# Kernel optimization log

Hardware: AMD Instinct MI355X
Metric: run time of the kernel (lower is better)

The kernel has to match this reference:

```python
import jax, jax.numpy as jnp
import numpy as np

VOXEL_SIZE = 0.4
PC_START = jnp.array([-75.2, -75.2], dtype=jnp.float32)
GAMMA = 1.1
RADII = (0.8, 1.6)
NSAMPLES = (16, 32)


def _sq_dist(a, b):
    # a:[N,3], b:[N,3] -> [N,N] squared distances (no [N,N,3] intermediate)
    sa = jnp.sum(a * a, axis=-1)
    sb = jnp.sum(b * b, axis=-1)
    return jnp.maximum(sa[:, None] + sb[None, :] - 2.0 * (a @ b.T), 0.0)


def _ball_group(d2, valid, pts, r, k):
    # CUDA ball_query semantics: first-k in-radius neighbor indices (index order),
    # empty slots padded with the first found index (0 if none).
    N = d2.shape[0]
    mask = (d2 < r * r) & valid[None, :]
    skey = jnp.where(mask, jnp.arange(N, dtype=jnp.int32)[None, :], N)
    idx = jnp.sort(skey, axis=-1)[:, :k]            # [N,k]
    first = idx[:, :1]
    idx = jnp.where(idx == N, first, idx)
    idx = jnp.where(idx == N, 0, idx)
    grouped_xyz = pts[idx, :3] - pts[:, None, :3]   # [N,k,3] relative xyz
    return jnp.concatenate([grouped_xyz, pts[idx, 3:5]], axis=-1)  # [N,k,5] (use_xyz)


def _mlp(x, ws, bs):
    for w, b in zip(ws, bs):
        x = jax.nn.relu(x @ w.T + b)
    return x


def _frame(pts, boxes, mlps, num_sample):
    # pts: [N,5] (x,y,z,intensity,time); boxes: [M,7]
    xy = pts[:, :2]
    coords = jnp.floor((xy - PC_START) / VOXEL_SIZE)              # per-point voxel xy coord
    qcoords = jnp.floor((boxes[:, :2] - PC_START) / VOXEL_SIZE)   # box voxel coords
    half_diag = jnp.linalg.norm(boxes[:, 3:5] * 0.5, axis=-1)
    rad_vox = jnp.ceil(half_diag * GAMMA / VOXEL_SIZE)
    dvox = jnp.abs(qcoords[:, None, :] - coords[None, :, :])      # [M,N,2]
    valid = jnp.any(jnp.all(dvox < rad_vox[:, None, None], axis=-1), axis=0)  # [N]

    # cylindrical_pool: per-box top-k points inside cylinder radius
    cur_radiis = half_diag * GAMMA
    dis = jnp.linalg.norm(boxes[:, None, :2] - xy[None, :, :], axis=-1)  # [M,N]
    point_mask = (dis <= cur_radiis[:, None]) & valid[None, :]
    sampled_mask, sampled_idx = jax.lax.top_k(point_mask.astype(pts.dtype), num_sample)

    # PointNet++ SA-MSG evaluated at every point (equivalent to unique->gather in torch src)
    d2 = _sq_dist(pts[:, :3], pts[:, :3])
    feats = [pts[:, :3]]  # use_absolute_xyz: concat query xyz first
    for r, k, (ws, bs) in zip(RADII, NSAMPLES, mlps):
        g = _ball_group(d2, valid, pts, r, k)
        feats.append(jnp.max(_mlp(g, ws, bs), axis=1))  # max-pool over neighbors
    feats = jnp.concatenate(feats, axis=-1)             # [N, 3+32+64]

    sampled_points = pts[sampled_idx] * sampled_mask[..., None]  # zero out-of-radius slots
    return sampled_points, feats[sampled_idx]


def _forward(points, trajectory_rois, params, num_sample):
    B, T, N, C = points.shape
    M = trajectory_rois.shape[2]
    sp, pf = jax.vmap(lambda p, b: _frame(p, b, params, num_sample))(
        points.reshape(B * T, N, C), trajectory_rois.reshape(B * T, M, -1))

    def _merge(x):
        x = x.reshape(B, T, M, num_sample, x.shape[-1])
        return x.transpose(0, 2, 1, 3, 4).reshape(B, M, T * num_sample, x.shape[-1])

    return _merge(sp), _merge(pf)


def setup_inputs():
    key = jax.random.key(0)
    ks = jax.random.split(key, 24)
    B, T, N, M = 2, 4, 4096, 128
    xy = jax.random.uniform(ks[0], (B, T, N, 2), minval=-74.0, maxval=74.0)
    z = jax.random.uniform(ks[1], (B, T, N, 1), minval=-2.0, maxval=4.0)
    inten = jax.random.uniform(ks[2], (B, T, N, 1))
    ts = jnp.broadcast_to(jnp.arange(T, dtype=jnp.float32)[None, :, None, None] * 0.1, (B, T, N, 1))
    points = jnp.concatenate([xy, z, inten, ts], axis=-1)
    bxy = jax.random.uniform(ks[3], (B, T, M, 2), minval=-70.0, maxval=70.0)
    bz = jax.random.uniform(ks[4], (B, T, M, 1), minval=-1.0, maxval=1.0)
    bdxy = jax.random.uniform(ks[5], (B, T, M, 2), minval=1.5, maxval=5.0)
    bdz = jax.random.uniform(ks[6], (B, T, M, 1), minval=1.0, maxval=2.0)
    bh = jax.random.uniform(ks[7], (B, T, M, 1), minval=0.0, maxval=6.28)
    trajectory_rois = jnp.concatenate([bxy, bz, bdxy, bdz, bh], axis=-1)
    inp = {"points": points, "trajectory_rois": trajectory_rois}
    dims = [("w00", 16, 5), ("w01", 16, 16), ("w02", 32, 16),
            ("w10", 32, 5), ("w11", 32, 32), ("w12", 64, 32)]
    for i, (nm, o, ic) in enumerate(dims):
        inp[nm] = jax.random.normal(ks[8 + i], (o, ic), dtype=jnp.float32) / np.sqrt(ic)
        inp["b" + nm[1:]] = jnp.zeros((o,), dtype=jnp.float32)
    inp["num_sample"] = 32
    return inp


def reference(points, trajectory_rois, w00, b00, w01, b01, w02, b02,
              w10, b10, w11, b11, w12, b12, num_sample):
    params = (((w00, w01, w02), (b00, b01, b02)),
              ((w10, w11, w12), (b10, b11, b12)))
    return _forward(points, trajectory_rois, params, num_sample)
```

## Files before the change

### kernel.cpp

```cpp
#include <hip/hip_runtime.h>
#include <hip/hip_bf16.h>
#include <stdint.h>

#define NFRM 8
#define NPTS 4096
#define NBOX 128
#define NS   32
#define TT   4
#define BB   2
#define FEATC 99
#define OUT1OFF (BB*NBOX*TT*NS*5)

#define WS_SPK    0u
#define WS_EPK    524288u
#define WS_FEATS  786432u
#define WS_SIDX   13762560u
#define WS_FLAGS  13893632u
#define WS_NCNT   14024704u
#define WS_NLST   14024736u
#define WS_VPK    14155808u
#define WS_VEK    14680096u
#define WS_VORIG  14942240u
#define WS_VCNT   15073312u
#define WS_WT     15073344u

__global__ void k_prep(const float* __restrict__ pts, const float* __restrict__ rois,
                       float4* __restrict__ spk, float2* __restrict__ epk,
                       const float* __restrict__ w00,const float* __restrict__ w01,
                       const float* __restrict__ w02,const float* __restrict__ w10,
                       const float* __restrict__ w11,const float* __restrict__ w12,
                       float* __restrict__ wt, int* __restrict__ flags,
                       int* __restrict__ gcnt)
{
    if (blockIdx.x == 128){
        int t = threadIdx.x;
        if (t == 0) *gcnt = 0;
        for (int idx=t; idx<80;   idx+=256){ int o=idx/5,  i=idx%5;  wt[      i*16+o]=w00[idx]; }
        for (int idx=t; idx<256;  idx+=256){ int o=idx/16, i=idx%16; wt[  80+ i*16+o]=w01[idx]; }
        for (int idx=t; idx<512;  idx+=256){ int o=idx/16, i=idx%16; wt[ 336+ i*32+o]=w02[idx]; }
        for (int idx=t; idx<160;  idx+=256){ int o=idx/5,  i=idx%5;  wt[ 848+ i*32+o]=w10[idx]; }
        for (int idx=t; idx<1024; idx+=256){ int o=idx/32, i=idx%32; wt[1008+ i*32+o]=w11[idx]; }
        for (int idx=t; idx<2048; idx+=256){ int o=idx/32, i=idx%32; wt[2032+ i*64+o]=w12[idx]; }
        return;
    }
    int f = blockIdx.x >> 4;
    int n = ((blockIdx.x & 15) << 8) | threadIdx.x;
    __shared__ float bqx[NBOX], bqy[NBOX], brv[NBOX];
    if (threadIdx.x < NBOX){
        const float* bp = rois + (size_t)(f*NBOX + threadIdx.x)*7;
        float bx=bp[0], by=bp[1], dx=bp[3], dy=bp[4];
        float hx=__fmul_rn(dx,0.5f), hy=__fmul_rn(dy,0.5f);
        float hd=sqrtf(__fadd_rn(__fmul_rn(hx,hx),__fmul_rn(hy,hy)));
        brv[threadIdx.x]=ceilf(__fdiv_rn(__fmul_rn(hd,1.1f),0.4f));
        bqx[threadIdx.x]=floorf(__fdiv_rn(__fsub_rn(bx,-75.2f),0.4f));
        bqy[threadIdx.x]=floorf(__fdiv_rn(__fsub_rn(by,-75.2f),0.4f));
    }
    flags[f*NPTS+n] = 0;
    __syncthreads();
    const float* pp = pts + (size_t)(f*NPTS+n)*5;
    float x=pp[0], y=pp[1], z=pp[2], it=pp[3], ts=pp[4];
    float cx=floorf(__fdiv_rn(__fsub_rn(x,-75.2f),0.4f));
    float cy=floorf(__fdiv_rn(__fsub_rn(y,-75.2f),0.4f));
    float v=0.f;
    for (int m=0;m<NBOX;m++)
        if (fabsf(bqx[m]-cx)<brv[m] && fabsf(bqy[m]-cy)<brv[m]){ v=1.f; break; }
    spk[f*NPTS+n]=make_float4(x,y,z,v);
    epk[f*NPTS+n]=make_float2(it,ts);
}

__global__ __launch_bounds__(1024) void k_valid(
    const float4* __restrict__ spk, const float2* __restrict__ epk,
    float4* __restrict__ vpk, float2* __restrict__ vek,
    int* __restrict__ vorig, int* __restrict__ vcnt)
{
    int f = blockIdx.x;
    int tid = threadIdx.x, wv = tid >> 6, lane = tid & 63;
    __shared__ int wcnt[16];
    __shared__ int sbase;
    if (tid == 0) sbase = 0;
    __syncthreads();
    uint64_t below = (1ull<<lane)-1ull;
    for (int j0=0; j0<NPTS; j0+=1024){
        int j = j0 + tid;
        float4 q = spk[f*NPTS+j];
        float2 e = epk[f*NPTS+j];
        bool pred = q.w > 0.5f;
        uint64_t m = __ballot(pred);
        int lp = __popcll(m & below);
        if (lane == 0) wcnt[wv] = __popcll(m);
        __syncthreads();
        int off = sbase;
        for (int w=0; w<wv; w++) off += wcnt[w];
        if (pred){
            int pos = off + lp;
            float sb = __fadd_rn(__fadd_rn(__fmul_rn(q.x,q.x),__fmul_rn(q.y,q.y)),__fmul_rn(q.z,q.z));
            vpk[f*NPTS+pos] = make_float4(q.x,q.y,q.z,sb);
            vek[f*NPTS+pos] = e;
            vorig[f*NPTS+pos] = j;
        }
        __syncthreads();
        if (tid == 0){ int t=0; for (int w=0;w<16;w++) t+=wcnt[w]; sbase += t; }
        __syncthreads();
    }
    if (tid == 0) vcnt[f] = sbase;
}

__global__ void k_select(const float4* __restrict__ spk, const float2* __restrict__ epk,
                         const float4* __restrict__ vpk, const int* __restrict__ vorig,
                         const int* __restrict__ vcnt,
                         const float* __restrict__ rois, float* __restrict__ out,
                         int* __restrict__ sidx, int* __restrict__ flags,
                         int* __restrict__ gcnt, int* __restrict__ glist)
{
    int id = blockIdx.x;
    int f = id >> 7, m = id & 127;
    int lane = threadIdx.x;
    const float* bp = rois + (size_t)(f*NBOX+m)*7;
    float bx=bp[0], by=bp[1], dx=bp[3], dy=bp[4];
    float hx=__fmul_rn(dx,0.5f), hy=__fmul_rn(dy,0.5f);
    float hd=sqrtf(__fadd_rn(__fmul_rn(hx,hx),__fmul_rn(hy,hy)));
    float rr=__fmul_rn(hd,1.1f);

    __shared__ int lt[32], lf[32];
    const float4* fsp = spk + f*NPTS;
    const float4* fvp = vpk + f*NPTS;
    const int*    fvo = vorig + f*NPTS;
    int vc = vcnt[f];
    uint64_t below = (1ull<<lane)-1ull;

    int cT=0;
    for (int v0=0; v0<vc; v0+=128){
        int viA = v0 + lane;
        int viB = v0 + 64 + lane;
        int vicA = min(viA, vc-1);
        int vicB = min(viB, vc-1);
        float4 qA = fvp[vicA];
        float4 qB = fvp[vicB];
        {
            float ddx=__fsub_rn(bx,qA.x), ddy=__fsub_rn(by,qA.y);
            float dis=sqrtf(__fadd_rn(__fmul_rn(ddx,ddx),__fmul_rn(ddy,ddy)));
            bool pm = (viA < vc) && (dis <= rr);
            uint64_t mT=__ballot(pm);
            if (pm){ int pos=cT+__popcll(mT&below); if (pos<32) lt[pos]=fvo[vicA]; }
            cT += __popcll(mT);
            if (cT>=32) break;
        }
        if (v0 + 64 < vc){
            float ddx=__fsub_rn(bx,qB.x), ddy=__fsub_rn(by,qB.y);
            float dis=sqrtf(__fadd_rn(__fmul_rn(ddx,ddx),__fmul_rn(ddy,ddy)));
            bool pm = (viB < vc) && (dis <= rr);
            uint64_t mT=__ballot(pm);
            if (pm){ int pos=cT+__popcll(mT&below); if (pos<32) lt[pos]=fvo[vicB]; }
            cT += __popcll(mT);
            if (cT>=32) break;
        }
    }
    int cF=0;
    for (int j0=0; j0<NPTS; j0+=64){
        int j=j0+lane;
        float4 q = fsp[j];
        float ddx=__fsub_rn(bx,q.x), ddy=__fsub_rn(by,q.y);
        float dis=sqrtf(__fadd_rn(__fmul_rn(ddx,ddx),__fmul_rn(ddy,ddy)));
        bool fl = !((dis <= rr) && (q.w > 0.5f));
        uint64_t mF=__ballot(fl);
        if (fl){ int pos=cF+__popcll(mF&below); if (pos<32) lf[pos]=j; }
        cF += __popcll(mF);
        if (cF>=32) break;
    }
    __syncthreads();
    cT = min(cT,32);
    if (lane < 32){
        int s = lane;
        bool masked = s < cT;
        int idx = masked ? lt[s] : lf[s-cT];
        float mk = masked ? 1.f : 0.f;
        sidx[(f*NBOX+m)*NS+s]=idx;
        int b = f >> 2, t = f & 3;
        size_t row = (((size_t)(b*NBOX+m))*TT + t)*NS + s;
        float4 q = fsp[idx]; float2 e = epk[f*NPTS+idx];
        float* o0 = out + row*5;
        o0[0]=q.x*mk; o0[1]=q.y*mk; o0[2]=q.z*mk; o0[3]=e.x*mk; o0[4]=e.y*mk;
        int old = atomicExch(&flags[f*NPTS+idx], 1);
        bool fresh = (old == 0);
        uint64_t mm = __ballot(fresh);
        if (fresh){
            int ldr = __ffsll((unsigned long long)mm) - 1;
            int base = 0;
            if (lane == ldr) base = atomicAdd(gcnt, __popcll(mm));
            base = __shfl(base, ldr);
            glist[base + __popcll(mm & below)] = (f<<12) | idx;
        }
    }
}

__global__ __launch_bounds__(256) void k_mlp(
    const float4* __restrict__ spk, const float2* __restrict__ epk,
    const float4* __restrict__ vpk, const float2* __restrict__ vek,
    const int* __restrict__ vcnt,
    const int* __restrict__ gcntp, const int* __restrict__ glist,
    float* __restrict__ feats, const float* __restrict__ wt,
    const float* __restrict__ b00,const float* __restrict__ b01,
    const float* __restrict__ b02,const float* __restrict__ b10,
    const float* __restrict__ b11,const float* __restrict__ b12)
{
    int gcnt = *gcntp;
    if ((int)blockIdx.x * 4 >= gcnt) return;
    int tid = threadIdx.x;
    int wv = tid >> 6, lane = tid & 63;
    __shared__ int lists[4][48];
    __shared__ float h1buf[4][4][36];
    __shared__ float h2buf[4][4][36];
    int* l1 = lists[wv];
    int* l2 = lists[wv]+16;
    float (*h1b)[36] = h1buf[wv];
    float (*h2b)[36] = h2buf[wv];

    float wr00[5], wr01[16], wr02[16], wr10[5], wr11[32], wr12[32];
    float br00=0.f, br01=0.f, br02=0.f, br10=0.f, br11=0.f, br12=0.f;
    #pragma unroll
    for (int i=0;i<5;i++){ wr00[i]=0.f; wr10[i]=0.f; }
    #pragma unroll
    for (int i=0;i<16;i++){ wr01[i]=0.f; wr02[i]=0.f; }
    #pragma unroll
    for (int i=0;i<32;i++){ wr11[i]=0.f; wr12[i]=0.f; }
    if (lane < 16){
        #pragma unroll
        for (int i=0;i<5;i++)  wr00[i]=wt[i*16+lane];
        br00=b00[lane];
        #pragma unroll
        for (int i=0;i<16;i++) wr01[i]=wt[80+i*16+lane];
        br01=b01[lane];
    }
    if (lane < 32){
        #pragma unroll
        for (int i=0;i<16;i++) wr02[i]=wt[336+i*32+lane];
        br02=b02[lane];
        #pragma unroll
        for (int i=0;i<5;i++)  wr10[i]=wt[848+i*32+lane];
        br10=b10[lane];
        #pragma unroll
        for (int i=0;i<32;i++) wr11[i]=wt[1008+i*32+lane];
        br11=b11[lane];
    }
    #pragma unroll
    for (int i=0;i<32;i++) wr12[i]=wt[2032+i*64+lane];
    br12=b12[lane];

    const float RR1 = (float)(0.8*0.8);
    const float RR2 = (float)(1.6*1.6);
    uint64_t below = (1ull<<lane)-1ull;

    for (int li = blockIdx.x*4 + wv; li < gcnt; li += 8192){
        int pe = glist[li];
        int f = pe >> 12, n = pe & 4095;
        const float4* fsp = spk + f*NPTS;
        const float2* fep = epk + f*NPTS;
        const float4* fvp = vpk + f*NPTS;
        const float2* fve = vek + f*NPTS;
        int vc = vcnt[f];
        float4 me = fsp[n];
        float sa = __fadd_rn(__fadd_rn(__fmul_rn(me.x,me.x),__fmul_rn(me.y,me.y)),__fmul_rn(me.z,me.z));

        int cnt1=0, cnt2=0;
        for (int v0=0; v0<vc; v0+=64){
            int vi = v0 + lane;
            int vic = min(vi, vc-1);
            float4 q = fvp[vic];
            float dot = __fadd_rn(__fadd_rn(__fmul_rn(me.x,q.x),__fmul_rn(me.y,q.y)),__fmul_rn(me.z,q.z));
            float d2 = fmaxf(__fsub_rn(__fadd_rn(sa,q.w),__fmul_rn(2.0f,dot)), 0.f);
            bool inb = (vi < vc);
            bool p1 = inb && (d2 < RR1);
            bool p2 = inb && (d2 < RR2);
            uint64_t m1 = __ballot(p1), m2 = __ballot(p2);
            if (p1){ int pos = cnt1 + __popcll(m1 & below); if (pos < 16) l1[pos] = vi; }
            if (p2){ int pos = cnt2 + __popcll(m2 & below); if (pos < 32) l2[pos] = vi; }
            cnt1 += __popcll(m1); cnt2 += __popcll(m2);
            if (cnt1 >= 16 && cnt2 >= 32) break;
        }
        cnt1 = min(cnt1,16); cnt2 = min(cnt2,32);

        float* fo = feats + (size_t)(f*NPTS+n)*FEATC;
        float4 q0 = fsp[0]; float2 e0 = fep[0];

        {
            float pmax = 0.f;
            #pragma unroll 1
            for (int kb=0; kb<16; kb+=4){
                float4 qb[4]; float2 eb[4];
                #pragma unroll
                for (int j=0;j<4;j++){
                    int kk = kb+j;
                    int vi = (cnt1>0) ? ((kk<cnt1)? l1[kk] : l1[0]) : -1;
                    if (vi >= 0){ qb[j]=fvp[vi]; eb[j]=fve[vi]; }
                    else        { qb[j]=q0;      eb[j]=e0; }
                }
                #pragma unroll
                for (int j=0;j<4;j++){
                    float a1 = br00;
                    a1 += __fsub_rn(qb[j].x,me.x)*wr00[0];
                    a1 += __fsub_rn(qb[j].y,me.y)*wr00[1];
                    a1 += __fsub_rn(qb[j].z,me.z)*wr00[2];
                    a1 += eb[j].x*wr00[3];
                    a1 += eb[j].y*wr00[4];
                    float h = fmaxf(a1,0.f);
                    if (lane < 16) h1b[j][lane] = h;
                }
                float a2[4] = {br01,br01,br01,br01};
                #pragma unroll
                for (int c4=0;c4<4;c4++){
                    float4 hv[4];
                    #pragma unroll
                    for (int j=0;j<4;j++) hv[j] = *(const float4*)&h1b[j][c4*4];
                    #pragma unroll
                    for (int cc=0;cc<4;cc++){
                        float w = wr01[c4*4+cc];
                        #pragma unroll
                        for (int j=0;j<4;j++){
                            float h = (cc==0)?hv[j].x:(cc==1)?hv[j].y:(cc==2)?hv[j].z:hv[j].w;
                            a2[j] += h*w;
                        }
                    }
                }
                #pragma unroll
                for (int j=0;j<4;j++){
                    float h = fmaxf(a2[j],0.f);
                    if (lane < 16) h2b[j][lane] = h;
                }
                float a3[4] = {br02,br02,br02,br02};
                #pragma unroll
                for (int c4=0;c4<4;c4++){
                    float4 hv[4];
                    #pragma unroll
                    for (int j=0;j<4;j++) hv[j] = *(const float4*)&h2b[j][c4*4];
                    #pragma unroll
                    for (int cc=0;cc<4;cc++){
                        float w = wr02[c4*4+cc];
                        #pragma unroll
                        for (int j=0;j<4;j++){
                            float h = (cc==0)?hv[j].x:(cc==1)?hv[j].y:(cc==2)?hv[j].z:hv[j].w;
                            a3[j] += h*w;
                        }
                    }
                }
                #pragma unroll
                for (int j=0;j<4;j++) pmax = fmaxf(pmax, fmaxf(a3[j],0.f));
            }
            if (lane < 3){
                float mv = (lane==0)? me.x : ((lane==1)? me.y : me.z);
                fo[lane] = mv;
            }
            if (lane < 32) fo[3+lane] = pmax;
        }

        {
            float pmax = 0.f;
            #pragma unroll 1
            for (int kb=0; kb<32; kb+=4){
                float4 qb[4]; float2 eb[4];
                #pragma unroll
                for (int j=0;j<4;j++){
                    int kk = kb+j;
                    int vi = (cnt2>0) ? ((kk<cnt2)? l2[kk] : l2[0]) : -1;
                    if (vi >= 0){ qb[j]=fvp[vi]; eb[j]=fve[vi]; }
                    else        { qb[j]=q0;      eb[j]=e0; }
                }
                #pragma unroll
                for (int j=0;j<4;j++){
                    float a1 = br10;
                    a1 += __fsub_rn(qb[j].x,me.x)*wr10[0];
                    a1 += __fsub_rn(qb[j].y,me.y)*wr10[1];
                    a1 += __fsub_rn(qb[j].z,me.z)*wr10[2];
                    a1 += eb[j].x*wr10[3];
                    a1 += eb[j].y*wr10[4];
                    float h = fmaxf(a1,0.f);
                    if (lane < 32) h1b[j][lane] = h;
                }
                float a2[4] = {br11,br11,br11,br11};
                #pragma unroll
                for (int c4=0;c4<8;c4++){
                    float4 hv[4];
                    #pragma unroll
                    for (int j=0;j<4;j++) hv[j] = *(const float4*)&h1b[j][c4*4];
                    #pragma unroll
                    for (int cc=0;cc<4;cc++){
                        float w = wr11[c4*4+cc];
                        #pragma unroll
                        for (int j=0;j<4;j++){
                            float h = (cc==0)?hv[j].x:(cc==1)?hv[j].y:(cc==2)?hv[j].z:hv[j].w;
                            a2[j] += h*w;
                        }
                    }
                }
                #pragma unroll
                for (int j=0;j<4;j++){
                    float h = fmaxf(a2[j],0.f);
                    if (lane < 32) h2b[j][lane] = h;
                }
                float a3[4] = {br12,br12,br12,br12};
                #pragma unroll
                for (int c4=0;c4<8;c4++){
                    float4 hv[4];
                    #pragma unroll
                    for (int j=0;j<4;j++) hv[j] = *(const float4*)&h2b[j][c4*4];
                    #pragma unroll
                    for (int cc=0;cc<4;cc++){
                        float w = wr12[c4*4+cc];
                        #pragma unroll
                        for (int j=0;j<4;j++){
                            float h = (cc==0)?hv[j].x:(cc==1)?hv[j].y:(cc==2)?hv[j].z:hv[j].w;
                            a3[j] += h*w;
                        }
                    }
                }
                #pragma unroll
                for (int j=0;j<4;j++) pmax = fmaxf(pmax, fmaxf(a3[j],0.f));
            }
            fo[35+lane] = pmax;
        }
    }
}

__global__ void k_gather(const float* __restrict__ feats, const int* __restrict__ sidx,
                         float* __restrict__ out)
{
    int id = blockIdx.x;
    int f = id >> 7, m = id & 127;
    int tid = threadIdx.x;
    int s = tid >> 3, j = tid & 7;
    int idx = sidx[(f*NBOX+m)*NS+s];
    int b = f >> 2, t = f & 3;
    size_t row = (((size_t)(b*NBOX+m))*TT + t)*NS + s;
    const float* fi = feats + (size_t)(f*NPTS+idx)*FEATC;
    float* o1 = out + OUT1OFF + row*FEATC;
    for (int c=j; c<FEATC; c+=8) o1[c]=fi[c];
}

extern "C" void kernel_launch(void* const* d_in, const int* in_sizes, int n_in,
                              void* d_out, int out_size, void* d_ws, size_t ws_size,
                              hipStream_t stream)
{
    const float* pts  = (const float*)d_in[0];
    const float* rois = (const float*)d_in[1];
    const float* w00=(const float*)d_in[2],  *b00=(const float*)d_in[3];
    const float* w01=(const float*)d_in[4],  *b01=(const float*)d_in[5];
    const float* w02=(const float*)d_in[6],  *b02=(const float*)d_in[7];
    const float* w10=(const float*)d_in[8],  *b10=(const float*)d_in[9];
    const float* w11=(const float*)d_in[10], *b11=(const float*)d_in[11];
    const float* w12=(const float*)d_in[12], *b12=(const float*)d_in[13];
    float* out = (float*)d_out;

    char* ws = (char*)d_ws;
    float4* spk   = (float4*)(ws + WS_SPK);
    float2* epk   = (float2*)(ws + WS_EPK);
    float*  feats = (float*) (ws + WS_FEATS);
    int*    sidx  = (int*)   (ws + WS_SIDX);
    int*    flags = (int*)   (ws + WS_FLAGS);
    int*    gcnt  = (int*)   (ws + WS_NCNT);
    int*    glist = (int*)   (ws + WS_NLST);
    float4* vpk   = (float4*)(ws + WS_VPK);
    float2* vek   = (float2*)(ws + WS_VEK);
    int*    vorig = (int*)   (ws + WS_VORIG);
    int*    vcnt  = (int*)   (ws + WS_VCNT);
    float*  wtr   = (float*) (ws + WS_WT);

    hipLaunchKernelGGL(k_prep,   dim3(NFRM*16+1), dim3(256), 0, stream,
                       pts, rois, spk, epk, w00,w01,w02,w10,w11,w12, wtr, flags, gcnt);
    hipLaunchKernelGGL(k_valid,  dim3(NFRM), dim3(1024), 0, stream, spk, epk, vpk, vek, vorig, vcnt);
    hipLaunchKernelGGL(k_select, dim3(NFRM*NBOX), dim3(64), 0, stream,
                       spk, epk, vpk, vorig, vcnt, rois, out, sidx, flags, gcnt, glist);
    hipLaunchKernelGGL(k_mlp,    dim3(2048), dim3(256), 0, stream,
                       spk, epk, vpk, vek, vcnt, gcnt, glist, feats, wtr,
                       b00,b01,b02,b10,b11,b12);
    hipLaunchKernelGGL(k_gather, dim3(NFRM*NBOX), dim3(256), 0, stream,
                       feats, sidx, out);
}
```

Before: 98.75 us.

## Split each point's MLP neighbors across four waves of a block

Previously each of the four waves in a block handled its own query point end to end, running the ball query and all 16+32 neighbor MLP evaluations serially. Now one block handles one point. Wave 0 runs the ball query, unrolled to 128 candidates per step, and shares the neighbor lists through LDS. All four waves then split the neighbor MLP work, and their partial max-pools are reduced through shared memory. The grid grows to 6144 blocks. This shortens the per-point serial chain and raises parallelism, at the cost of three __syncthreads per point and three idle waves during the ball query.

```diff
diff --git a/kernel.cpp b/kernel.cpp
--- a/kernel.cpp
+++ b/kernel.cpp
@@ -204,14 +204,17 @@
     const float* __restrict__ b11,const float* __restrict__ b12)
 {
     int gcnt = *gcntp;
-    if ((int)blockIdx.x * 4 >= gcnt) return;
+    if ((int)blockIdx.x >= gcnt) return;
     int tid = threadIdx.x;
     int wv = tid >> 6, lane = tid & 63;
-    __shared__ int lists[4][48];
+    __shared__ int slst[48];
+    __shared__ int scn[2];
     __shared__ float h1buf[4][4][36];
     __shared__ float h2buf[4][4][36];
-    int* l1 = lists[wv];
-    int* l2 = lists[wv]+16;
+    __shared__ float p0[3][32];
+    __shared__ float p1[3][64];
+    int* l1 = slst;
+    int* l2 = slst+16;
     float (*h1b)[36] = h1buf[wv];
     float (*h2b)[36] = h2buf[wv];
 
@@ -250,7 +253,7 @@
     const float RR2 = (float)(1.6*1.6);
     uint64_t below = (1ull<<lane)-1ull;
 
-    for (int li = blockIdx.x*4 + wv; li < gcnt; li += 8192){
+    for (int li = blockIdx.x; li < gcnt; li += gridDim.x){
         int pe = glist[li];
         int f = pe >> 12, n = pe & 4095;
         const float4* fsp = spk + f*NPTS;
@@ -261,162 +264,191 @@
         float4 me = fsp[n];
         float sa = __fadd_rn(__fadd_rn(__fmul_rn(me.x,me.x),__fmul_rn(me.y,me.y)),__fmul_rn(me.z,me.z));
 
-        int cnt1=0, cnt2=0;
-        for (int v0=0; v0<vc; v0+=64){
-            int vi = v0 + lane;
-            int vic = min(vi, vc-1);
-            float4 q = fvp[vic];
-            float dot = __fadd_rn(__fadd_rn(__fmul_rn(me.x,q.x),__fmul_rn(me.y,q.y)),__fmul_rn(me.z,q.z));
-            float d2 = fmaxf(__fsub_rn(__fadd_rn(sa,q.w),__fmul_rn(2.0f,dot)), 0.f);
-            bool inb = (vi < vc);
-            bool p1 = inb && (d2 < RR1);
-            bool p2 = inb && (d2 < RR2);
-            uint64_t m1 = __ballot(p1), m2 = __ballot(p2);
-            if (p1){ int pos = cnt1 + __popcll(m1 & below); if (pos < 16) l1[pos] = vi; }
-            if (p2){ int pos = cnt2 + __popcll(m2 & below); if (pos < 32) l2[pos] = vi; }
-            cnt1 += __popcll(m1); cnt2 += __popcll(m2);
-            if (cnt1 >= 16 && cnt2 >= 32) break;
-        }
-        cnt1 = min(cnt1,16); cnt2 = min(cnt2,32);
+        if (wv == 0){
+            int cnt1=0, cnt2=0;
+            for (int v0=0; v0<vc; v0+=128){
+                int viA = v0 + lane;
+                int viB = v0 + 64 + lane;
+                int vicA = min(viA, vc-1);
+                int vicB = min(viB, vc-1);
+                float4 qA = fvp[vicA];
+                float4 qB = fvp[vicB];
+                {
+                    float dot = __fadd_rn(__fadd_rn(__fmul_rn(me.x,qA.x),__fmul_rn(me.y,qA.y)),__fmul_rn(me.z,qA.z));
+                    float d2 = fmaxf(__fsub_rn(__fadd_rn(sa,qA.w),__fmul_rn(2.0f,dot)), 0.f);
+                    bool inb = (viA < vc);
+                    bool p1b = inb && (d2 < RR1);
+                    bool p2b = inb && (d2 < RR2);
+                    uint64_t m1 = __ballot(p1b), m2 = __ballot(p2b);
+                    if (p1b){ int pos = cnt1 + __popcll(m1 & below); if (pos < 16) l1[pos] = viA; }
+                    if (p2b){ int pos = cnt2 + __popcll(m2 & below); if (pos < 32) l2[pos] = viA; }
+                    cnt1 += __popcll(m1); cnt2 += __popcll(m2);
+                    if (cnt1 >= 16 && cnt2 >= 32) break;
+                }
+                if (v0 + 64 < vc){
+                    float dot = __fadd_rn(__fadd_rn(__fmul_rn(me.x,qB.x),__fmul_rn(me.y,qB.y)),__fmul_rn(me.z,qB.z));
+                    float d2 = fmaxf(__fsub_rn(__fadd_rn(sa,qB.w),__fmul_rn(2.0f,dot)), 0.f);
+                    bool inb = (viB < vc);
+                    bool p1b = inb && (d2 < RR1);
+                    bool p2b = inb && (d2 < RR2);
+                    uint64_t m1 = __ballot(p1b), m2 = __ballot(p2b);
+                    if (p1b){ int pos = cnt1 + __popcll(m1 & below); if (pos < 16) l1[pos] = viB; }
+                    if (p2b){ int pos = cnt2 + __popcll(m2 & below); if (pos < 32) l2[pos] = viB; }
+                    cnt1 += __popcll(m1); cnt2 += __popcll(m2);
+                    if (cnt1 >= 16 && cnt2 >= 32) break;
+                }
+            }
+            if (lane == 0){ scn[0] = min(cnt1,16); scn[1] = min(cnt2,32); }
+        }
+        __syncthreads();
+        int cnt1 = scn[0], cnt2 = scn[1];
 
         float* fo = feats + (size_t)(f*NPTS+n)*FEATC;
         float4 q0 = fsp[0]; float2 e0 = fep[0];
 
+        float pm0;
         {
-            float pmax = 0.f;
-            #pragma unroll 1
-            for (int kb=0; kb<16; kb+=4){
-                float4 qb[4]; float2 eb[4];
-                #pragma unroll
-                for (int j=0;j<4;j++){
-                    int kk = kb+j;
-                    int vi = (cnt1>0) ? ((kk<cnt1)? l1[kk] : l1[0]) : -1;
-                    if (vi >= 0){ qb[j]=fvp[vi]; eb[j]=fve[vi]; }
-                    else        { qb[j]=q0;      eb[j]=e0; }
-                }
-                #pragma unroll
-                for (int j=0;j<4;j++){
-                    float a1 = br00;
-                    a1 += __fsub_rn(qb[j].x,me.x)*wr00[0];
-                    a1 += __fsub_rn(qb[j].y,me.y)*wr00[1];
-                    a1 += __fsub_rn(qb[j].z,me.z)*wr00[2];
-                    a1 += eb[j].x*wr00[3];
-                    a1 += eb[j].y*wr00[4];
-                    float h = fmaxf(a1,0.f);
-                    if (lane < 16) h1b[j][lane] = h;
-                }
-                float a2[4] = {br01,br01,br01,br01};
-                #pragma unroll
-                for (int c4=0;c4<4;c4++){
-                    float4 hv[4];
+            float4 qb[4]; float2 eb[4];
+            #pragma unroll
+            for (int j=0;j<4;j++){
+                int kk = wv + 4*j;
+                int vi = (cnt1>0) ? ((kk<cnt1)? l1[kk] : l1[0]) : -1;
+                if (vi >= 0){ qb[j]=fvp[vi]; eb[j]=fve[vi]; }
+                else        { qb[j]=q0;      eb[j]=e0; }
+            }
+            #pragma unroll
+            for (int j=0;j<4;j++){
+                float a1 = br00;
+                a1 += __fsub_rn(qb[j].x,me.x)*wr00[0];
+                a1 += __fsub_rn(qb[j].y,me.y)*wr00[1];
+                a1 += __fsub_rn(qb[j].z,me.z)*wr00[2];
+                a1 += eb[j].x*wr00[3];
+                a1 += eb[j].y*wr00[4];
+                float h = fmaxf(a1,0.f);
+                if (lane < 16) h1b[j][lane] = h;
+            }
+            float a2[4] = {br01,br01,br01,br01};
+            #pragma unroll
+            for (int c4=0;c4<4;c4++){
+                float4 hv[4];
+                #pragma unroll
+                for (int j=0;j<4;j++) hv[j] = *(const float4*)&h1b[j][c4*4];
+                #pragma unroll
+                for (int cc=0;cc<4;cc++){
+                    float w = wr01[c4*4+cc];
                     #pragma unroll
-                    for (int j=0;j<4;j++) hv[j] = *(const float4*)&h1b[j][c4*4];
-                    #pragma unroll
-                    for (int cc=0;cc<4;cc++){
-                        float w = wr01[c4*4+cc];
-                        #pragma unroll
-                        for (int j=0;j<4;j++){
-                            float h = (cc==0)?hv[j].x:(cc==1)?hv[j].y:(cc==2)?hv[j].z:hv[j].w;
-                            a2[j] += h*w;
-                        }
+                    for (int j=0;j<4;j++){
+                        float h = (cc==0)?hv[j].x:(cc==1)?hv[j].y:(cc==2)?hv[j].z:hv[j].w;
+                        a2[j] += h*w;
                     }
                 }
-                #pragma unroll
-                for (int j=0;j<4;j++){
-                    float h = fmaxf(a2[j],0.f);
-                    if (lane < 16) h2b[j][lane] = h;
-                }
-                float a3[4] = {br02,br02,br02,br02};
-                #pragma unroll
-                for (int c4=0;c4<4;c4++){
-                    float4 hv[4];
+            }
+            #pragma unroll
+            for (int j=0;j<4;j++){
+                float h = fmaxf(a2[j],0.f);
+                if (lane < 16) h2b[j][lane] = h;
+            }
+            float a3[4] = {br02,br02,br02,br02};
+            #pragma unroll
+            for (int c4=0;c4<4;c4++){
+                float4 hv[4];
+                #pragma unroll
+                for (int j=0;j<4;j++) hv[j] = *(const float4*)&h2b[j][c4*4];
+                #pragma unroll
+                for (int cc=0;cc<4;cc++){
+                    float w = wr02[c4*4+cc];
                     #pragma unroll
-                    for (int j=0;j<4;j++) hv[j] = *(const float4*)&h2b[j][c4*4];
-                    #pragma unroll
-                    for (int cc=0;cc<4;cc++){
-                        float w = wr02[c4*4+cc];
-                        #pragma unroll
-                        for (int j=0;j<4;j++){
-                            float h = (cc==0)?hv[j].x:(cc==1)?hv[j].y:(cc==2)?hv[j].z:hv[j].w;
-                            a3[j] += h*w;
-                        }
+                    for (int j=0;j<4;j++){
+                        float h = (cc==0)?hv[j].x:(cc==1)?hv[j].y:(cc==2)?hv[j].z:hv[j].w;
+                        a3[j] += h*w;
                     }
                 }
-                #pragma unroll
-                for (int j=0;j<4;j++) pmax = fmaxf(pmax, fmaxf(a3[j],0.f));
-            }
+            }
+            pm0 = fmaxf(fmaxf(fmaxf(a3[0],0.f), fmaxf(a3[1],0.f)),
+                        fmaxf(fmaxf(a3[2],0.f), fmaxf(a3[3],0.f)));
+        }
+
+        float pm1 = 0.f;
+        #pragma unroll 1
+        for (int jb=0; jb<8; jb+=4){
+            float4 qb[4]; float2 eb[4];
+            #pragma unroll
+            for (int j=0;j<4;j++){
+                int kk = wv + 4*(jb+j);
+                int vi = (cnt2>0) ? ((kk<cnt2)? l2[kk] : l2[0]) : -1;
+                if (vi >= 0){ qb[j]=fvp[vi]; eb[j]=fve[vi]; }
+                else        { qb[j]=q0;      eb[j]=e0; }
+            }
+            #pragma unroll
+            for (int j=0;j<4;j++){
+                float a1 = br10;
+                a1 += __fsub_rn(qb[j].x,me.x)*wr10[0];
+                a1 += __fsub_rn(qb[j].y,me.y)*wr10[1];
+                a1 += __fsub_rn(qb[j].z,me.z)*wr10[2];
+                a1 += eb[j].x*wr10[3];
+                a1 += eb[j].y*wr10[4];
+                float h = fmaxf(a1,0.f);
+                if (lane < 32) h1b[j][lane] = h;
+            }
+            float a2[4] = {br11,br11,br11,br11};
+            #pragma unroll
+            for (int c4=0;c4<8;c4++){
+                float4 hv[4];
+                #pragma unroll
+                for (int j=0;j<4;j++) hv[j] = *(const float4*)&h1b[j][c4*4];
+                #pragma unroll
+                for (int cc=0;cc<4;cc++){
+                    float w = wr11[c4*4+cc];
+                    #pragma unroll
+                    for (int j=0;j<4;j++){
+                        float h = (cc==0)?hv[j].x:(cc==1)?hv[j].y:(cc==2)?hv[j].z:hv[j].w;
+                        a2[j] += h*w;
+                    }
+                }
+            }
+            #pragma unroll
+            for (int j=0;j<4;j++){
+                float h = fmaxf(a2[j],0.f);
+                if (lane < 32) h2b[j][lane] = h;
+            }
+            float a3[4] = {br12,br12,br12,br12};
+            #pragma unroll
+            for (int c4=0;c4<8;c4++){
+                float4 hv[4];
+                #pragma unroll
+                for (int j=0;j<4;j++) hv[j] = *(const float4*)&h2b[j][c4*4];
+                #pragma unroll
+                for (int cc=0;cc<4;cc++){
+                    float w = wr12[c4*4+cc];
+                    #pragma unroll
+                    for (int j=0;j<4;j++){
+                        float h = (cc==0)?hv[j].x:(cc==1)?hv[j].y:(cc==2)?hv[j].z:hv[j].w;
+                        a3[j] += h*w;
+                    }
+                }
+            }
+            #pragma unroll
+            for (int j=0;j<4;j++) pm1 = fmaxf(pm1, fmaxf(a3[j],0.f));
+        }
+
+        if (wv > 0){
+            if (lane < 32) p0[wv-1][lane] = pm0;
+            p1[wv-1][lane] = pm1;
+        }
+        __syncthreads();
+        if (wv == 0){
+            float r0 = fmaxf(fmaxf(pm0, p0[0][lane & 31]),
+                             fmaxf(p0[1][lane & 31], p0[2][lane & 31]));
+            float r1 = fmaxf(fmaxf(pm1, p1[0][lane]),
+                             fmaxf(p1[1][lane], p1[2][lane]));
             if (lane < 3){
                 float mv = (lane==0)? me.x : ((lane==1)? me.y : me.z);
                 fo[lane] = mv;
             }
-            if (lane < 32) fo[3+lane] = pmax;
-        }
-
-        {
-            float pmax = 0.f;
-            #pragma unroll 1
-            for (int kb=0; kb<32; kb+=4){
-                float4 qb[4]; float2 eb[4];
-                #pragma unroll
-                for (int j=0;j<4;j++){
-                    int kk = kb+j;
-                    int vi = (cnt2>0) ? ((kk<cnt2)? l2[kk] : l2[0]) : -1;
-                    if (vi >= 0){ qb[j]=fvp[vi]; eb[j]=fve[vi]; }
-                    else        { qb[j]=q0;      eb[j]=e0; }
-                }
-                #pragma unroll
-                for (int j=0;j<4;j++){
-                    float a1 = br10;
-                    a1 += __fsub_rn(qb[j].x,me.x)*wr10[0];
-                    a1 += __fsub_rn(qb[j].y,me.y)*wr10[1];
-                    a1 += __fsub_rn(qb[j].z,me.z)*wr10[2];
-                    a1 += eb[j].x*wr10[3];
-                    a1 += eb[j].y*wr10[4];
-                    float h = fmaxf(a1,0.f);
-                    if (lane < 32) h1b[j][lane] = h;
-                }
-                float a2[4] = {br11,br11,br11,br11};
-                #pragma unroll
-                for (int c4=0;c4<8;c4++){
-                    float4 hv[4];
-                    #pragma unroll
-                    for (int j=0;j<4;j++) hv[j] = *(const float4*)&h1b[j][c4*4];
-                    #pragma unroll
-                    for (int cc=0;cc<4;cc++){
-                        float w = wr11[c4*4+cc];
-                        #pragma unroll
-                        for (int j=0;j<4;j++){
-                            float h = (cc==0)?hv[j].x:(cc==1)?hv[j].y:(cc==2)?hv[j].z:hv[j].w;
-                            a2[j] += h*w;
-                        }
-                    }
-                }
-                #pragma unroll
-                for (int j=0;j<4;j++){
-                    float h = fmaxf(a2[j],0.f);
-                    if (lane < 32) h2b[j][lane] = h;
-                }
-                float a3[4] = {br12,br12,br12,br12};
-                #pragma unroll
-                for (int c4=0;c4<8;c4++){
-                    float4 hv[4];
-                    #pragma unroll
-                    for (int j=0;j<4;j++) hv[j] = *(const float4*)&h2b[j][c4*4];
-                    #pragma unroll
-                    for (int cc=0;cc<4;cc++){
-                        float w = wr12[c4*4+cc];
-                        #pragma unroll
-                        for (int j=0;j<4;j++){
-                            float h = (cc==0)?hv[j].x:(cc==1)?hv[j].y:(cc==2)?hv[j].z:hv[j].w;
-                            a3[j] += h*w;
-                        }
-                    }
-                }
-                #pragma unroll
-                for (int j=0;j<4;j++) pmax = fmaxf(pmax, fmaxf(a3[j],0.f));
-            }
-            fo[35+lane] = pmax;
-        }
+            if (lane < 32) fo[3+lane] = r0;
+            fo[35+lane] = r1;
+        }
+        __syncthreads();
     }
 }
 
@@ -468,7 +500,7 @@
     hipLaunchKernelGGL(k_valid,  dim3(NFRM), dim3(1024), 0, stream, spk, epk, vpk, vek, vorig, vcnt);
     hipLaunchKernelGGL(k_select, dim3(NFRM*NBOX), dim3(64), 0, stream,
                        spk, epk, vpk, vorig, vcnt, rois, out, sidx, flags, gcnt, glist);
-    hipLaunchKernelGGL(k_mlp,    dim3(2048), dim3(256), 0, stream,
+    hipLaunchKernelGGL(k_mlp,    dim3(6144), dim3(256), 0, stream,
                        spk, epk, vpk, vek, vcnt, gcnt, glist, feats, wtr,
                        b00,b01,b02,b10,b11,b12);
     hipLaunchKernelGGL(k_gather, dim3(NFRM*NBOX), dim3(256), 0, stream,
```

Result: slower. 121.5 us (+23.0%).
